# Optimization experiments

Measured on AMD Instinct MI355X. Metric: run time of the kernel, lower is better.

## Reference

```python
import jax, jax.numpy as jnp
import numpy as np

ALPHA = 1.0
MIN_FEATURE_SIZE = 1.0
SC = 1e-12
EPS_V_FLOOR = 1e-32 ** (1.0 / 6.0)  # ~4.64e-6, floor on gradient magnitude


def setup_inputs() -> dict:
    key = jax.random.key(0)
    eps = jax.random.normal(key, (8192, 8192), dtype=jnp.float32)
    grid_size = jnp.asarray(0.05, dtype=jnp.float32)
    return {"eps": eps, "grid_size": grid_size}


def _ls_derivatives(phi, d):
    # torch.gradient == numpy.gradient with edge_order=1 (central interior, one-sided edges)
    phi_x, phi_y = jnp.gradient(phi, d, d)
    phi_x = phi_x + SC
    phi_y = phi_y + SC
    phi_xx, phi_xy = jnp.gradient(phi_x, d, d)        # second derivs of phi_x
    phi_yy = jnp.gradient(phi_y, d, axis=1)           # only d/dy of phi_y is used
    return phi_x, phi_y, phi_xx, phi_xy, phi_yy


def reference(eps, grid_size):
    ex, ey, exx, exy, eyy = _ls_derivatives(eps, grid_size)
    pi_d = jnp.pi / (1.1 * MIN_FEATURE_SIZE)
    eps_v = jnp.maximum(jnp.sqrt(ex * ex + ey * ey), jnp.float32(EPS_V_FLOOR))
    k = (ex * ex * eyy - 2.0 * ex * ey * exy + ey * ey * exx) / (eps_v ** 3)
    curve_const = jnp.abs(k * jnp.arctan(eps_v / (eps + 1e-6))) - pi_d
    return jnp.nansum(ALPHA * jnp.maximum(curve_const, 0.0) * grid_size ** 2)
```

## Files before the change

kernel.cpp:

```cpp
#include <hip/hip_runtime.h>
#include <math.h>


typedef float f2 __attribute__((ext_vector_type(2)));
typedef float f4 __attribute__((ext_vector_type(4)));

constexpr float SCF = 1e-12f;
constexpr float EVF = 4.6415888336e-6f;
constexpr float PID = 2.8559933214452666f;
constexpr float PIH = 1.5707963268f;
constexpr int   RS  = 64;
constexpr int   FT  = 40;

struct Row { f4 lo, hi; };

__device__ __forceinline__ float C(const Row& r, int k) {
    return k < 4 ? r.lo[k] : r.hi[k - 4];
}
__device__ __forceinline__ void load_row(Row& r, const float* p) {
    r.lo = *(const f4*)p;
    r.hi = *(const f4*)(p + 4);
}
__device__ __forceinline__ f2 mk(float a, float b) { f2 v; v.x = a; v.y = b; return v; }
__device__ __forceinline__ f2 fma2(f2 a, f2 b, f2 c) { return __builtin_elementwise_fma(a, b, c); }
__device__ __forceinline__ f2 max2(f2 a, f2 b) { return __builtin_elementwise_max(a, b); }
__device__ __forceinline__ f2 min2(f2 a, f2 b) { return __builtin_elementwise_min(a, b); }
__device__ __forceinline__ f2 abs2(f2 a) { return __builtin_elementwise_abs(a); }
__device__ __forceinline__ f2 rcp2(f2 a) {
    return mk(__builtin_amdgcn_rcpf(a.x), __builtin_amdgcn_rcpf(a.y));
}
__device__ __forceinline__ f2 rsq2(f2 a) {
    return mk(__builtin_amdgcn_rsqf(a.x), __builtin_amdgcn_rsqf(a.y));
}

__device__ __forceinline__ f2 compute_pair(const Row& R0, const Row& R1,
                                           const Row& R2, const Row& R3,
                                           const Row& R4, const Row& R5,
                                           f2 c1, f2 c2) {
    f2 dif[6];
    #pragma unroll
    for (int k = 0; k < 6; ++k)
        dif[k] = mk(C(R3, k + 1) - C(R1, k + 1),
                    C(R4, k + 1) - C(R2, k + 1));
    f2 Pz[8];
    #pragma unroll
    for (int k = 0; k < 8; ++k)
        Pz[k] = mk(C(R2, k), C(R3, k));

    f2 part = mk(0.0f, 0.0f);
    #pragma unroll
    for (int q = 0; q < 4; ++q) {
        const f2 c00  = Pz[q + 2];
        const f2 u    = dif[q + 1];
        const f2 v    = Pz[q + 3] - Pz[q + 1];
        const f2 exxr = fma2(mk(-2.0f, -2.0f), c00,
                             mk(C(R4, q + 2) + C(R0, q + 2),
                                C(R5, q + 2) + C(R1, q + 2)));
        const f2 eyyr = fma2(mk(-2.0f, -2.0f), c00, Pz[q + 4] + Pz[q]);
        const f2 exyr = dif[q + 2] - dif[q];

        const f2 uu  = u * u;
        const f2 vv  = v * v;
        const f2 r2  = uu + vv;
        const f2 rsq = rsq2(r2);
        const f2 N   = fma2(uu, eyyr, fma2(-2.0f * (u * v), exyr, vv * exxr));
        const f2 r3  = rsq * rsq * rsq;
        const f2 kabs = abs2(N) * min2(c1 * r3, c2);
        const f2 ev   = max2(c1 * (r2 * rsq), mk(EVF, EVF));

        const f2 aw = abs2(c00 + 1e-6f);
        const f2 mx = max2(ev, aw);
        const f2 mn = min2(ev, aw);
        const f2 t  = mn * rcp2(mx);
        const f2 t2 = t * t;
        f2 pl = fma2(t2, mk(-0.01172120f, -0.01172120f), mk(0.05265332f, 0.05265332f));
        pl = fma2(t2, pl, mk(-0.11643287f, -0.11643287f));
        pl = fma2(t2, pl, mk(0.19354346f, 0.19354346f));
        pl = fma2(t2, pl, mk(-0.33262347f, -0.33262347f));
        pl = fma2(t2, pl, mk(0.99997726f, 0.99997726f));
        pl = pl * t;
        f2 at;
        at.x = (ev.x > aw.x) ? PIH - pl.x : pl.x;
        at.y = (ev.y > aw.y) ? PIH - pl.y : pl.y;

        part = part + max2(fma2(kabs, at, mk(-PID, -PID)), mk(0.0f, 0.0f));
    }
    return part;
}

__device__ __forceinline__ float penalty_scalar(float ex, float ey, float exx,
                                                float exy, float eyy, float w) {
    const float ev = fmaxf(__builtin_amdgcn_sqrtf(fmaf(ex, ex, ey * ey)), EVF);
    const float num = fmaf(ex * ex, eyy, fmaf(-2.0f * ex * ey, exy, ey * ey * exx));
    const float kabs = fabsf(num) * __builtin_amdgcn_rcpf(ev * ev * ev);
    const float aw = fabsf(w + 1e-6f);
    const float mx = fmaxf(ev, aw);
    const float mn = fminf(ev, aw);
    const float t  = mn * __builtin_amdgcn_rcpf(mx);
    const float t2 = t * t;
    float pl = fmaf(t2, -0.01172120f, 0.05265332f);
    pl = fmaf(t2, pl, -0.11643287f);
    pl = fmaf(t2, pl, 0.19354346f);
    pl = fmaf(t2, pl, -0.33262347f);
    pl = fmaf(t2, pl, 0.99997726f);
    pl *= t;
    const float at = (ev > aw) ? (PIH - pl) : pl;
    return fmaxf(fmaf(kabs, at, -PID), 0.0f);
}

__device__ __forceinline__ float eg(const float* __restrict__ e, int n, int i, int j) {
    return e[(size_t)i * (size_t)n + j];
}
__device__ __forceinline__ float gex(const float* __restrict__ e, int n, int i, int j,
                                     float inv_d, float inv_2d) {
    float v;
    if (i == 0)          v = (eg(e, n, 1, j) - eg(e, n, 0, j)) * inv_d;
    else if (i == n - 1) v = (eg(e, n, n - 1, j) - eg(e, n, n - 2, j)) * inv_d;
    else                 v = (eg(e, n, i + 1, j) - eg(e, n, i - 1, j)) * inv_2d;
    return v + SCF;
}
__device__ __forceinline__ float gey(const float* __restrict__ e, int n, int i, int j,
                                     float inv_d, float inv_2d) {
    float v;
    if (j == 0)          v = (eg(e, n, i, 1) - eg(e, n, i, 0)) * inv_d;
    else if (j == n - 1) v = (eg(e, n, i, n - 1) - eg(e, n, i, n - 2)) * inv_d;
    else                 v = (eg(e, n, i, j + 1) - eg(e, n, i, j - 1)) * inv_2d;
    return v + SCF;
}

__global__ __launch_bounds__(256, 4)
void fab_fused(const float* __restrict__ eps, const float* __restrict__ gs,
               float* __restrict__ ws, int n, int G2) {
    const float d      = *gs;
    const float inv_2d = 0.5f / d;
    const float inv_d  = inv_2d + inv_2d;
    const float c1s    = inv_2d;
    const float c2s    = 1e16f * (inv_2d * inv_2d) * (inv_2d * inv_2d);
    const int bflat    = blockIdx.y * gridDim.x + blockIdx.x;

    float acc = 0.0f;

    if (threadIdx.x < FT) {
        const int t = bflat * FT + (int)threadIdx.x;
        const int ntop = 4 * n;
        if (t < ntop) {
            const int rr = (t >= n) + (t >= 2 * n) + (t >= 3 * n);
            const int j = t - rr * n;
            const int i = (rr < 2) ? rr : (n - 4) + rr;

            const float ex0 = gex(eps, n, i, j, inv_d, inv_2d);
            const float ey0 = gey(eps, n, i, j, inv_d, inv_2d);
            float exx, exy, eyy;
            if (i == 0)
                exx = (gex(eps, n, 1, j, inv_d, inv_2d) - ex0) * inv_d;
            else if (i == n - 1)
                exx = (ex0 - gex(eps, n, n - 2, j, inv_d, inv_2d)) * inv_d;
            else
                exx = (gex(eps, n, i + 1, j, inv_d, inv_2d)
                     - gex(eps, n, i - 1, j, inv_d, inv_2d)) * inv_2d;
            if (j == 0)
                exy = (gex(eps, n, i, 1, inv_d, inv_2d) - ex0) * inv_d;
            else if (j == n - 1)
                exy = (ex0 - gex(eps, n, i, n - 2, inv_d, inv_2d)) * inv_d;
            else
                exy = (gex(eps, n, i, j + 1, inv_d, inv_2d)
                     - gex(eps, n, i, j - 1, inv_d, inv_2d)) * inv_2d;
            if (j == 0)
                eyy = (gey(eps, n, i, 1, inv_d, inv_2d) - ey0) * inv_d;
            else if (j == n - 1)
                eyy = (ey0 - gey(eps, n, i, n - 2, inv_d, inv_2d)) * inv_d;
            else
                eyy = (gey(eps, n, i, j + 1, inv_d, inv_2d)
                     - gey(eps, n, i, j - 1, inv_d, inv_2d)) * inv_2d;

            acc += penalty_scalar(ex0, ey0, exx, exy, eyy, eg(eps, n, i, j));
        } else if (t < ntop + (n - 4)) {
            const int i = 2 + (t - ntop);
            float W[5][12];
            const float* rb = eps + (size_t)(i - 2) * (size_t)n;
            #pragma unroll
            for (int r = 0; r < 5; ++r) {
                const f4 a = *(const f4*)(rb + (size_t)r * n);
                const f4 b = *(const f4*)(rb + (size_t)r * n + (n - 8));
                const f4 c = *(const f4*)(rb + (size_t)r * n + (n - 4));
                #pragma unroll
                for (int k = 0; k < 4; ++k) {
                    W[r][k] = a[k]; W[r][4 + k] = b[k]; W[r][8 + k] = c[k];
                }
            }
            auto exW = [&](int r, int wc) {
                return (W[r + 1][wc] - W[r - 1][wc]) * inv_2d + SCF;
            };
            auto eyW = [&](int wc) {
                if (wc == 0)  return (W[2][1] - W[2][0]) * inv_d + SCF;
                if (wc == 11) return (W[2][11] - W[2][10]) * inv_d + SCF;
                return (W[2][wc + 1] - W[2][wc - 1]) * inv_2d + SCF;
            };
            #pragma unroll
            for (int m = 0; m < 8; ++m) {
                const int wc = (m < 2) ? m : m + 4;
                const float ex0 = exW(2, wc);
                const float ey0 = eyW(wc);
                const float exx = (exW(3, wc) - exW(1, wc)) * inv_2d;
                float exy, eyy;
                if (wc == 0) {
                    exy = (exW(2, 1) - exW(2, 0)) * inv_d;
                    eyy = (eyW(1) - eyW(0)) * inv_d;
                } else if (wc == 11) {
                    exy = (exW(2, 11) - exW(2, 10)) * inv_d;
                    eyy = (eyW(11) - eyW(10)) * inv_d;
                } else {
                    exy = (exW(2, wc + 1) - exW(2, wc - 1)) * inv_2d;
                    eyy = (eyW(wc + 1) - eyW(wc - 1)) * inv_2d;
                }
                acc += penalty_scalar(ex0, ey0, exx, exy, eyy, W[2][wc]);
            }
        }
    }

    {
        const int gg = blockIdx.x * 256 + threadIdx.x;
        const bool valid = gg < G2;
        const int gc = min(gg, G2 - 1);
        const int i0 = 2 + RS * blockIdx.y;
        const int count = min(RS, (n - 2) - i0);
        const float* pj = eps + 4 * (size_t)gc;
        const size_t sn = (size_t)n;
        const f2 c1 = mk(c1s, c1s);
        const f2 c2 = mk(c2s, c2s);

        f2 acc2 = mk(0.0f, 0.0f);

        auto sweep = [&](int start, int len) {
            Row s0, s1, s2, s3, s4, s5, s6, s7;
            load_row(s0, pj + (size_t)(start - 2) * sn);
            load_row(s1, pj + (size_t)(start - 1) * sn);
            load_row(s2, pj + (size_t)(start    ) * sn);
            load_row(s3, pj + (size_t)(start + 1) * sn);
            load_row(s4, pj + (size_t)(start + 2) * sn);
            load_row(s5, pj + (size_t)(start + 3) * sn);
            const float* pnext = pj + (size_t)(start + 4) * sn;

            #define PHASEP(ph, A0, A1, A2, A3, A4, A5, L0, L1)                \
            {                                                                 \
                const int k = kbase + 2 * (ph);                               \
                if (k < len) {                                                \
                    if (k + 2 < len) {                                        \
                        load_row(L0, pnext);                                  \
                        load_row(L1, pnext + sn);                             \
                    }                                                         \
                    pnext += 2 * sn;                                          \
                    acc2 = acc2 + compute_pair(A0, A1, A2, A3, A4, A5,        \
                                               c1, c2);                       \
                }                                                             \
            }
            #pragma unroll 1
            for (int kbase = 0; kbase < len; kbase += 8) {
                PHASEP(0, s0, s1, s2, s3, s4, s5, s6, s7)
                PHASEP(1, s2, s3, s4, s5, s6, s7, s0, s1)
                PHASEP(2, s4, s5, s6, s7, s0, s1, s2, s3)
                PHASEP(3, s6, s7, s0, s1, s2, s3, s4, s5)
            }
            #undef PHASEP
        };

        const int off = 16 * (bflat & 3);
        sweep(i0 + off, count - off);
        if (off > 0) sweep(i0, off);

        if (valid) acc += acc2.x + acc2.y;
    }

    __shared__ float wsum[4];
    #pragma unroll
    for (int off = 32; off; off >>= 1)
        acc += __shfl_down(acc, off, 64);
    if ((threadIdx.x & 63) == 0) wsum[threadIdx.x >> 6] = acc;
    __syncthreads();
    if (threadIdx.x == 0)
        ws[bflat] = wsum[0] + wsum[1] + wsum[2] + wsum[3];
}

__global__ __launch_bounds__(256)
void fab_finish(const float* __restrict__ ws, const float* __restrict__ gs,
                float* __restrict__ out, int nb) {
    __shared__ float wsum[4];
    float v = 0.0f;
    for (int i = threadIdx.x; i < nb; i += 256) v += ws[i];
    #pragma unroll
    for (int off = 32; off; off >>= 1)
        v += __shfl_down(v, off, 64);
    if ((threadIdx.x & 63) == 0) wsum[threadIdx.x >> 6] = v;
    __syncthreads();
    if (threadIdx.x == 0) {
        const float d = *gs;
        out[0] = (wsum[0] + wsum[1] + wsum[2] + wsum[3]) * d * d;
    }
}

extern "C" void kernel_launch(void* const* d_in, const int* in_sizes, int n_in,
                              void* d_out, int out_size, void* d_ws, size_t ws_size,
                              hipStream_t stream) {
    const float* eps = (const float*)d_in[0];
    const float* gs  = (const float*)d_in[1];
    float* out = (float*)d_out;
    float* ws  = (float*)d_ws;

    const long long tot = (long long)in_sizes[0];
    const int n = (int)(sqrt((double)tot) + 0.5);

    const int G2 = (n - 8) / 4;
    const int nstrip = (n - 4 + RS - 1) / RS;

    dim3 block(256, 1);
    dim3 grid(n / 1024, nstrip);
    fab_fused<<<grid, block, 0, stream>>>(eps, gs, ws, n, G2);
    fab_finish<<<1, 256, 0, stream>>>(ws, gs, out, grid.x * grid.y);
}
```

Measured before the change: 85.29 us.

## Replace paired-row f2 stencil sweep with single-row rotating sweep and smaller strips

The column-strip stencil loop now computes one output row per step in scalar float, replacing two rows per step with packed f2 math. It uses a 6-register-row rotation instead of 8, and drops the staggered start offset across blocks. Strip height is halved (RS 64 to 32, FT 40 to 20) and launch bounds raised to 6 waves per SIMD. The goal is fewer registers, higher occupancy and more blocks, at the cost of more halo rereads per strip, losing packed-FP32 throughput, and no longer staggering DRAM access across blocks.

```diff
diff --git a/kernel.cpp b/kernel.cpp
--- a/kernel.cpp
+++ b/kernel.cpp
@@ -2,15 +2,14 @@
 #include <math.h>
 
 
-typedef float f2 __attribute__((ext_vector_type(2)));
 typedef float f4 __attribute__((ext_vector_type(4)));
 
 constexpr float SCF = 1e-12f;
 constexpr float EVF = 4.6415888336e-6f;
 constexpr float PID = 2.8559933214452666f;
 constexpr float PIH = 1.5707963268f;
-constexpr int   RS  = 64;
-constexpr int   FT  = 40;
+constexpr int   RS  = 32;
+constexpr int   FT  = 20;
 
 struct Row { f4 lo, hi; };
 
@@ -21,69 +20,49 @@
     r.lo = *(const f4*)p;
     r.hi = *(const f4*)(p + 4);
 }
-__device__ __forceinline__ f2 mk(float a, float b) { f2 v; v.x = a; v.y = b; return v; }
-__device__ __forceinline__ f2 fma2(f2 a, f2 b, f2 c) { return __builtin_elementwise_fma(a, b, c); }
-__device__ __forceinline__ f2 max2(f2 a, f2 b) { return __builtin_elementwise_max(a, b); }
-__device__ __forceinline__ f2 min2(f2 a, f2 b) { return __builtin_elementwise_min(a, b); }
-__device__ __forceinline__ f2 abs2(f2 a) { return __builtin_elementwise_abs(a); }
-__device__ __forceinline__ f2 rcp2(f2 a) {
-    return mk(__builtin_amdgcn_rcpf(a.x), __builtin_amdgcn_rcpf(a.y));
-}
-__device__ __forceinline__ f2 rsq2(f2 a) {
-    return mk(__builtin_amdgcn_rsqf(a.x), __builtin_amdgcn_rsqf(a.y));
-}
-
-__device__ __forceinline__ f2 compute_pair(const Row& R0, const Row& R1,
-                                           const Row& R2, const Row& R3,
-                                           const Row& R4, const Row& R5,
-                                           f2 c1, f2 c2) {
-    f2 dif[6];
+
+__device__ __forceinline__ float compute_row(const Row& R0, const Row& R1,
+                                             const Row& R2, const Row& R3,
+                                             const Row& R4,
+                                             float c1, float c2) {
+    float dif[6];
     #pragma unroll
     for (int k = 0; k < 6; ++k)
-        dif[k] = mk(C(R3, k + 1) - C(R1, k + 1),
-                    C(R4, k + 1) - C(R2, k + 1));
-    f2 Pz[8];
-    #pragma unroll
-    for (int k = 0; k < 8; ++k)
-        Pz[k] = mk(C(R2, k), C(R3, k));
-
-    f2 part = mk(0.0f, 0.0f);
+        dif[k] = C(R3, k + 1) - C(R1, k + 1);
+
+    float part = 0.0f;
     #pragma unroll
     for (int q = 0; q < 4; ++q) {
-        const f2 c00  = Pz[q + 2];
-        const f2 u    = dif[q + 1];
-        const f2 v    = Pz[q + 3] - Pz[q + 1];
-        const f2 exxr = fma2(mk(-2.0f, -2.0f), c00,
-                             mk(C(R4, q + 2) + C(R0, q + 2),
-                                C(R5, q + 2) + C(R1, q + 2)));
-        const f2 eyyr = fma2(mk(-2.0f, -2.0f), c00, Pz[q + 4] + Pz[q]);
-        const f2 exyr = dif[q + 2] - dif[q];
-
-        const f2 uu  = u * u;
-        const f2 vv  = v * v;
-        const f2 r2  = uu + vv;
-        const f2 rsq = rsq2(r2);
-        const f2 N   = fma2(uu, eyyr, fma2(-2.0f * (u * v), exyr, vv * exxr));
-        const f2 r3  = rsq * rsq * rsq;
-        const f2 kabs = abs2(N) * min2(c1 * r3, c2);
-        const f2 ev   = max2(c1 * (r2 * rsq), mk(EVF, EVF));
-
-        const f2 aw = abs2(c00 + 1e-6f);
-        const f2 mx = max2(ev, aw);
-        const f2 mn = min2(ev, aw);
-        const f2 t  = mn * rcp2(mx);
-        const f2 t2 = t * t;
-        f2 pl = fma2(t2, mk(-0.01172120f, -0.01172120f), mk(0.05265332f, 0.05265332f));
-        pl = fma2(t2, pl, mk(-0.11643287f, -0.11643287f));
-        pl = fma2(t2, pl, mk(0.19354346f, 0.19354346f));
-        pl = fma2(t2, pl, mk(-0.33262347f, -0.33262347f));
-        pl = fma2(t2, pl, mk(0.99997726f, 0.99997726f));
-        pl = pl * t;
-        f2 at;
-        at.x = (ev.x > aw.x) ? PIH - pl.x : pl.x;
-        at.y = (ev.y > aw.y) ? PIH - pl.y : pl.y;
-
-        part = part + max2(fma2(kabs, at, mk(-PID, -PID)), mk(0.0f, 0.0f));
+        const float c00  = C(R2, q + 2);
+        const float u    = dif[q + 1];
+        const float v    = C(R2, q + 3) - C(R2, q + 1);
+        const float exxr = fmaf(-2.0f, c00, C(R4, q + 2) + C(R0, q + 2));
+        const float eyyr = fmaf(-2.0f, c00, C(R2, q + 4) + C(R2, q));
+        const float exyr = dif[q + 2] - dif[q];
+
+        const float uu  = u * u;
+        const float vv  = v * v;
+        const float r2  = uu + vv;
+        const float rsq = __builtin_amdgcn_rsqf(r2);
+        const float N   = fmaf(uu, eyyr, fmaf(-2.0f * (u * v), exyr, vv * exxr));
+        const float r3  = rsq * rsq * rsq;
+        const float kabs = fabsf(N) * fminf(c1 * r3, c2);
+        const float ev   = fmaxf(c1 * (r2 * rsq), EVF);
+
+        const float aw = fabsf(c00 + 1e-6f);
+        const float mx = fmaxf(ev, aw);
+        const float mn = fminf(ev, aw);
+        const float t  = mn * __builtin_amdgcn_rcpf(mx);
+        const float t2 = t * t;
+        float pl = fmaf(t2, -0.01172120f, 0.05265332f);
+        pl = fmaf(t2, pl, -0.11643287f);
+        pl = fmaf(t2, pl, 0.19354346f);
+        pl = fmaf(t2, pl, -0.33262347f);
+        pl = fmaf(t2, pl, 0.99997726f);
+        pl *= t;
+        const float at = (ev > aw) ? (PIH - pl) : pl;
+
+        part += fmaxf(fmaf(kabs, at, -PID), 0.0f);
     }
     return part;
 }
@@ -128,14 +107,14 @@
     return v + SCF;
 }
 
-__global__ __launch_bounds__(256, 4)
+__global__ __launch_bounds__(256, 6)
 void fab_fused(const float* __restrict__ eps, const float* __restrict__ gs,
                float* __restrict__ ws, int n, int G2) {
     const float d      = *gs;
     const float inv_2d = 0.5f / d;
     const float inv_d  = inv_2d + inv_2d;
-    const float c1s    = inv_2d;
-    const float c2s    = 1e16f * (inv_2d * inv_2d) * (inv_2d * inv_2d);
+    const float c1     = inv_2d;
+    const float c2     = 1e16f * (inv_2d * inv_2d) * (inv_2d * inv_2d);
     const int bflat    = blockIdx.y * gridDim.x + blockIdx.x;
 
     float acc = 0.0f;
@@ -226,49 +205,38 @@
         const int count = min(RS, (n - 2) - i0);
         const float* pj = eps + 4 * (size_t)gc;
         const size_t sn = (size_t)n;
-        const f2 c1 = mk(c1s, c1s);
-        const f2 c2 = mk(c2s, c2s);
-
-        f2 acc2 = mk(0.0f, 0.0f);
-
-        auto sweep = [&](int start, int len) {
-            Row s0, s1, s2, s3, s4, s5, s6, s7;
-            load_row(s0, pj + (size_t)(start - 2) * sn);
-            load_row(s1, pj + (size_t)(start - 1) * sn);
-            load_row(s2, pj + (size_t)(start    ) * sn);
-            load_row(s3, pj + (size_t)(start + 1) * sn);
-            load_row(s4, pj + (size_t)(start + 2) * sn);
-            load_row(s5, pj + (size_t)(start + 3) * sn);
-            const float* pnext = pj + (size_t)(start + 4) * sn;
-
-            #define PHASEP(ph, A0, A1, A2, A3, A4, A5, L0, L1)                \
-            {                                                                 \
-                const int k = kbase + 2 * (ph);                               \
-                if (k < len) {                                                \
-                    if (k + 2 < len) {                                        \
-                        load_row(L0, pnext);                                  \
-                        load_row(L1, pnext + sn);                             \
-                    }                                                         \
-                    pnext += 2 * sn;                                          \
-                    acc2 = acc2 + compute_pair(A0, A1, A2, A3, A4, A5,        \
-                                               c1, c2);                       \
-                }                                                             \
-            }
-            #pragma unroll 1
-            for (int kbase = 0; kbase < len; kbase += 8) {
-                PHASEP(0, s0, s1, s2, s3, s4, s5, s6, s7)
-                PHASEP(1, s2, s3, s4, s5, s6, s7, s0, s1)
-                PHASEP(2, s4, s5, s6, s7, s0, s1, s2, s3)
-                PHASEP(3, s6, s7, s0, s1, s2, s3, s4, s5)
-            }
-            #undef PHASEP
-        };
-
-        const int off = 16 * (bflat & 3);
-        sweep(i0 + off, count - off);
-        if (off > 0) sweep(i0, off);
-
-        if (valid) acc += acc2.x + acc2.y;
+
+        Row s0, s1, s2, s3, s4, s5;
+        load_row(s0, pj + (size_t)(i0 - 2) * sn);
+        load_row(s1, pj + (size_t)(i0 - 1) * sn);
+        load_row(s2, pj + (size_t)(i0    ) * sn);
+        load_row(s3, pj + (size_t)(i0 + 1) * sn);
+        load_row(s4, pj + (size_t)(i0 + 2) * sn);
+        const float* pnext = pj + (size_t)(i0 + 3) * sn;
+
+        float accs = 0.0f;
+        #define PHASE1(ph, A0, A1, A2, A3, A4, LD)                            \
+        {                                                                     \
+            const int k = kbase + (ph);                                       \
+            if (k < count) {                                                  \
+                if (k + 2 <= count) load_row(LD, pnext);                      \
+                pnext += sn;                                                  \
+                accs += compute_row(A0, A1, A2, A3, A4, c1, c2);              \
+            }                                                                 \
+        }
+
+        #pragma unroll 1
+        for (int kbase = 0; kbase < RS; kbase += 6) {
+            PHASE1(0, s0, s1, s2, s3, s4, s5)
+            PHASE1(1, s1, s2, s3, s4, s5, s0)
+            PHASE1(2, s2, s3, s4, s5, s0, s1)
+            PHASE1(3, s3, s4, s5, s0, s1, s2)
+            PHASE1(4, s4, s5, s0, s1, s2, s3)
+            PHASE1(5, s5, s0, s1, s2, s3, s4)
+        }
+        #undef PHASE1
+
+        if (valid) acc += accs;
     }
 
     __shared__ float wsum[4];
```

Result: slower. 96.23 us, median of 2 (+12.8%).
